# Kernel tuning notes

Hardware: AMD Instinct MI355X
Metric: run time of the kernel (lower is better)

The kernel has to match this reference:

```python
import jax, jax.numpy as jnp
import numpy as np

D = 1024
B = 16
T = 2048
LN_EPS = 1e-5


def setup_inputs() -> dict:
    key = jax.random.key(0)
    k_x, k_in, k_st = jax.random.split(key, 3)
    x = jax.random.normal(k_x, (B, T, D), dtype=jnp.float32)
    # nn.Linear(d, 2d, bias=False): weight [2D, D], y = x @ W.T
    s_in = 1.0 / np.sqrt(D)
    W_in = jax.random.uniform(k_in, (2 * D, D), dtype=jnp.float32, minval=-s_in, maxval=s_in)
    W_state = jax.random.uniform(k_st, (D, D), dtype=jnp.float32, minval=-s_in, maxval=s_in)
    gamma = jnp.ones((D,), dtype=jnp.float32)
    beta = jnp.zeros((D,), dtype=jnp.float32)
    return {"x": x, "W_in": W_in, "W_state": W_state, "gamma": gamma, "beta": beta}


def _glru(x, W_in, W_state, gamma, beta):
    # Batched projections over all timesteps (gates depend only on x).
    proj = jnp.einsum("btd,ed->bte", x, W_in)            # [B, T, 2D]
    gx, vx = jnp.split(proj, 2, axis=-1)                   # each [B, T, D]
    u = jax.nn.sigmoid(gx)                                  # [B, T, D]
    cand = jnp.einsum("btd,ed->bte", vx, W_state)        # [B, T, D]

    # Sequential diagonal linear recurrence: h_t = u_t * h_{t-1} + (1-u_t)*cand_t
    def step(h, uc):
        u_t, c_t = uc
        h = u_t * h + (1.0 - u_t) * c_t
        return h, h

    h0 = jnp.zeros((x.shape[0], x.shape[2]), dtype=x.dtype)
    us = jnp.swapaxes(u, 0, 1)       # [T, B, D]
    cs = jnp.swapaxes(cand, 0, 1)    # [T, B, D]
    _, ys = jax.lax.scan(step, h0, (us, cs))
    y = jnp.swapaxes(ys, 0, 1)       # [B, T, D]

    # LayerNorm over last dim
    mu = jnp.mean(y, axis=-1, keepdims=True)
    var = jnp.mean(jnp.square(y - mu), axis=-1, keepdims=True)
    return (y - mu) * jax.lax.rsqrt(var + LN_EPS) * gamma + beta


def reference(x, W_in, W_state, gamma, beta):
    return _glru(x, W_in, W_state, gamma, beta)
```

## Files before the change

### kernel.cpp

```cpp
#include <hip/hip_runtime.h>

#define D_DIM 1024
#define B_DIM 16
#define T_DIM 2048
#define M_TOT (B_DIM * T_DIM)
#define K_DIM 1024
#define LN_EPS 1e-5f
#define CHUNK 16
#define NCH (T_DIM / CHUNK)

typedef _Float16 half8 __attribute__((ext_vector_type(8)));
typedef _Float16 half4v __attribute__((ext_vector_type(4)));
typedef float f32x4 __attribute__((ext_vector_type(4)));

__global__ __launch_bounds__(256) void cvt_f32_f16(const float* __restrict__ in,
                                                   _Float16* __restrict__ out, int n8) {
    int i = blockIdx.x * blockDim.x + threadIdx.x;
    int stride = gridDim.x * blockDim.x;
    for (; i < n8; i += stride) {
        const float4* p = (const float4*)in + 2 * (size_t)i;
        float4 a = p[0], b = p[1];
        half8 h;
        h[0] = (_Float16)a.x; h[1] = (_Float16)a.y; h[2] = (_Float16)a.z; h[3] = (_Float16)a.w;
        h[4] = (_Float16)b.x; h[5] = (_Float16)b.y; h[6] = (_Float16)b.z; h[7] = (_Float16)b.w;
        ((half8*)out)[i] = h;
    }
}

__global__ __launch_bounds__(256) void transpose_cvt(const float* __restrict__ in,
                                                     _Float16* __restrict__ out) {
    __shared__ _Float16 t[32][33];
    int bx = blockIdx.x * 32, by = blockIdx.y * 32;
    int tx = threadIdx.x, ty = threadIdx.y;
#pragma unroll
    for (int j = 0; j < 4; ++j)
        t[ty + 8 * j][tx] = (_Float16)in[(size_t)(by + ty + 8 * j) * 1024 + bx + tx];
    __syncthreads();
#pragma unroll
    for (int j = 0; j < 4; ++j)
        out[(size_t)(bx + ty + 8 * j) * 1024 + by + tx] = t[tx][ty + 8 * j];
}

__device__ __forceinline__ void gl_lds16(const _Float16* g, _Float16* l) {
    __builtin_amdgcn_global_load_lds(
        (const __attribute__((address_space(1))) unsigned int*)g,
        (__attribute__((address_space(3))) unsigned int*)l,
        16, 0, 0);
}


__device__ __forceinline__ void stageA32(const _Float16* __restrict__ G,
                                         int row0, int kt,
                                         _Float16* lds0, int wid, int lane) {
#pragma unroll
    for (int call = 0; call < 2; ++call) {
        int c0 = call * 256 + wid * 64;
        int c  = c0 + lane;
        int rl = c >> 2;
        int cc = c & 3;
        int src = cc ^ ((rl >> 1) & 3);
        gl_lds16(G + (size_t)(row0 + rl) * 1024 + kt + src * 8,
                 lds0 + (size_t)c0 * 8);
    }
}

__device__ __forceinline__ void stageB32(const _Float16* __restrict__ G,
                                         int row0, int kt,
                                         _Float16* lds0, int wid, int lane) {
#pragma unroll
    for (int call = 0; call < 4; ++call) {
        int c0 = call * 256 + wid * 64;
        int c  = c0 + lane;
        int rl = c >> 2;
        int cc = c & 3;
        int src = cc ^ ((rl >> 1) & 3);
        gl_lds16(G + (size_t)(row0 + rl) * 1024 + kt + src * 8,
                 lds0 + (size_t)c0 * 8);
    }
}

__device__ __forceinline__ half8 frag32(const _Float16* base, int row, int kq) {
    int cc = kq ^ ((row >> 1) & 3);
    return *(const half8*)(base + (size_t)row * 32 + cc * 8);
}

template <int TB>
__device__ __forceinline__ void gstep(const _Float16* __restrict__ A,
                                      const _Float16* __restrict__ W,
                                      int m0, int nrow0, int t, int nkt,
                                      int wid, int lane, int wc, int r, int kq,
                                      _Float16 (&As)[3][128][32],
                                      _Float16 (&Bs)[3][256][32],
                                      f32x4 (&acc)[8][4]) {
    constexpr int NB = (TB + 2) % 3;
    half8 rb[4], ra0[4], ra1[4];

    if (t + 1 < nkt) asm volatile("s_waitcnt vmcnt(6)" ::: "memory");
    else             asm volatile("s_waitcnt vmcnt(0)" ::: "memory");
    __builtin_amdgcn_s_barrier();
    __builtin_amdgcn_sched_barrier(0);

#pragma unroll
    for (int ni = 0; ni < 4; ni++) rb[ni]  = frag32(&Bs[TB][0][0], wc * 64 + ni * 16 + r, kq);
#pragma unroll
    for (int mi = 0; mi < 4; mi++) ra0[mi] = frag32(&As[TB][0][0], mi * 16 + r, kq);
    if (t + 2 < nkt) {
        int kt2 = (t + 2) << 5;
        stageA32(A, m0,    kt2, &As[NB][0][0], wid, lane);
        stageB32(W, nrow0, kt2, &Bs[NB][0][0], wid, lane);
    }
    __builtin_amdgcn_s_setprio(1);
#pragma unroll
    for (int mi = 0; mi < 4; mi++)
#pragma unroll
        for (int ni = 0; ni < 4; ni++)
            acc[mi][ni] = __builtin_amdgcn_mfma_f32_16x16x32_f16(ra0[mi], rb[ni], acc[mi][ni], 0, 0, 0);
    __builtin_amdgcn_s_setprio(0);

#pragma unroll
    for (int mi = 0; mi < 4; mi++) ra1[mi] = frag32(&As[TB][0][0], 64 + mi * 16 + r, kq);
    __builtin_amdgcn_s_setprio(1);
#pragma unroll
    for (int mi = 0; mi < 4; mi++)
#pragma unroll
        for (int ni = 0; ni < 4; ni++)
            acc[4 + mi][ni] = __builtin_amdgcn_mfma_f32_16x16x32_f16(ra1[mi], rb[ni], acc[4 + mi][ni], 0, 0, 0);
    __builtin_amdgcn_s_setprio(0);
    __builtin_amdgcn_s_barrier();
}

__global__ __launch_bounds__(256, 2) void gemm256(const _Float16* __restrict__ A,
                                                  const _Float16* __restrict__ W,
                                                  _Float16* __restrict__ out0,
                                                  _Float16* __restrict__ out1) {
    __shared__ _Float16 As[3][128][32];
    __shared__ _Float16 Bs[3][256][32];

    int bid = blockIdx.x;
    int xcd = bid & 7, lin = bid >> 3;
    int mt = xcd * 32 + (lin >> 3);
    int nt = lin & 7;
    int m0 = mt * 128, nrow0 = nt * 256;

    int tid = threadIdx.x, wid = tid >> 6, lane = tid & 63;
    int wc = wid;
    int r = lane & 15, kq = lane >> 4;

    f32x4 acc[8][4];
#pragma unroll
    for (int i = 0; i < 8; i++)
#pragma unroll
        for (int j = 0; j < 4; j++) acc[i][j] = (f32x4)0.f;

    const int nkt = K_DIM >> 5;

    stageA32(A, m0,    0,  &As[0][0][0], wid, lane);
    stageB32(W, nrow0, 0,  &Bs[0][0][0], wid, lane);
    stageA32(A, m0,    32, &As[1][0][0], wid, lane);
    stageB32(W, nrow0, 32, &Bs[1][0][0], wid, lane);

    for (int t0 = 0; t0 < nkt; t0 += 3) {
        gstep<0>(A, W, m0, nrow0, t0, nkt, wid, lane, wc, r, kq, As, Bs, acc);
        if (t0 + 1 < nkt)
            gstep<1>(A, W, m0, nrow0, t0 + 1, nkt, wid, lane, wc, r, kq, As, Bs, acc);
        if (t0 + 2 < nkt)
            gstep<2>(A, W, m0, nrow0, t0 + 2, nkt, wid, lane, wc, r, kq, As, Bs, acc);
    }

    bool isGate = (nt < 4);
    _Float16* dst = isGate ? out0 : out1;
    int cb = (nt & 3) * 256 + wc * 64;
    int rr = kq * 4;
#pragma unroll
    for (int mi = 0; mi < 8; mi++) {
        int mbase = m0 + mi * 16 + rr;
#pragma unroll
        for (int ni = 0; ni < 4; ni++) {
            int n = cb + ni * 16 + r;
#pragma unroll
            for (int q = 0; q < 4; q++) {
                float v = acc[mi][ni][q];
                if (isGate) v = 1.f / (1.f + __expf(-v));
                dst[(size_t)(mbase + q) * D_DIM + n] = (_Float16)v;
            }
        }
    }
}

__global__ __launch_bounds__(256) void wcomb_splitk(const _Float16* __restrict__ A,
                                                    const _Float16* __restrict__ Bm,
                                                    float* __restrict__ part) {
    __shared__ _Float16 As[128 * 32];
    __shared__ _Float16 Bs[128 * 32];
    int bid = blockIdx.x;
    int mt = bid & 7, nt = (bid >> 3) & 7, sl = bid >> 6;
    int m0 = mt * 128, n0 = nt * 128, kbeg = sl * 256;
    int tid = threadIdx.x, wid = tid >> 6, lane = tid & 63;
    int wr = wid >> 1, wc = wid & 1;

    f32x4 acc[4][4];
#pragma unroll
    for (int i = 0; i < 4; i++)
#pragma unroll
        for (int j = 0; j < 4; j++) acc[i][j] = (f32x4)0.f;

    int r = lane & 15, kq = lane >> 4;

    for (int kt = kbeg; kt < kbeg + 256; kt += 32) {
        __syncthreads();
#pragma unroll
        for (int j = 0; j < 2; ++j) {
            int f = j * 256 + tid;
            int row = f >> 2, kc = f & 3;
            gl_lds16(A + (size_t)(m0 + row) * 1024 + kt + kc * 8, As + (size_t)(j * 256 + wid * 64) * 8);
            gl_lds16(Bm + (size_t)(n0 + row) * 1024 + kt + kc * 8, Bs + (size_t)(j * 256 + wid * 64) * 8);
        }
        __syncthreads();
        half8 af[4], bf[4];
#pragma unroll
        for (int mi = 0; mi < 4; mi++) af[mi] = *(const half8*)&As[(wr * 64 + mi * 16 + r) * 32 + kq * 8];
#pragma unroll
        for (int ni = 0; ni < 4; ni++) bf[ni] = *(const half8*)&Bs[(wc * 64 + ni * 16 + r) * 32 + kq * 8];
#pragma unroll
        for (int mi = 0; mi < 4; mi++)
#pragma unroll
            for (int ni = 0; ni < 4; ni++)
                acc[mi][ni] = __builtin_amdgcn_mfma_f32_16x16x32_f16(af[mi], bf[ni], acc[mi][ni], 0, 0, 0);
    }

    int rr = kq * 4;
    float* pbp = part + (size_t)sl * 1048576;
#pragma unroll
    for (int mi = 0; mi < 4; mi++) {
        int mbase = m0 + wr * 64 + mi * 16 + rr;
#pragma unroll
        for (int ni = 0; ni < 4; ni++) {
            int n = n0 + wc * 64 + ni * 16 + r;
#pragma unroll
            for (int q = 0; q < 4; q++)
                pbp[(size_t)(mbase + q) * 1024 + n] = acc[mi][ni][q];
        }
    }
}

__global__ __launch_bounds__(256) void wcomb_combine(const float* __restrict__ part,
                                                     _Float16* __restrict__ out) {
    int i = blockIdx.x * 256 + threadIdx.x;
    float4 s0 = ((const float4*)part)[i];
    float4 s1 = ((const float4*)(part + 1048576))[i];
    float4 s2 = ((const float4*)(part + 2097152))[i];
    float4 s3 = ((const float4*)(part + 3145728))[i];
    half4v o;
    o[0] = (_Float16)(s0.x + s1.x + s2.x + s3.x);
    o[1] = (_Float16)(s0.y + s1.y + s2.y + s3.y);
    o[2] = (_Float16)(s0.z + s1.z + s2.z + s3.z);
    o[3] = (_Float16)(s0.w + s1.w + s2.w + s3.w);
    ((half4v*)out)[i] = o;
}

__global__ __launch_bounds__(256) void scan_pass1(const _Float16* __restrict__ u,
                                                  const _Float16* __restrict__ cd,
                                                  float* __restrict__ Ac, float* __restrict__ Bc) {
    int idx = blockIdx.x * 256 + threadIdx.x;
    int dg = idx & 127, bc = idx >> 7;
    int b = bc >> 7, ch = bc & (NCH - 1);
    int d0 = dg * 8;
    size_t base = ((size_t)b * T_DIM + (size_t)ch * CHUNK) * D_DIM + d0;
    float Aa[8], Bb[8];
#pragma unroll
    for (int j = 0; j < 8; ++j) { Aa[j] = 1.f; Bb[j] = 0.f; }
#pragma unroll
    for (int t = 0; t < CHUNK; ++t) {
        half8 u8 = *(const half8*)&u[base + (size_t)t * D_DIM];
        half8 c8 = *(const half8*)&cd[base + (size_t)t * D_DIM];
#pragma unroll
        for (int j = 0; j < 8; ++j) {
            float ut = (float)u8[j], ct = (float)c8[j];
            Aa[j] *= ut;
            Bb[j] = fmaf(ut, Bb[j], (1.f - ut) * ct);
        }
    }
    size_t o = (size_t)bc * D_DIM + d0;
    *(float4*)&Ac[o]     = *(float4*)&Aa[0];
    *(float4*)&Ac[o + 4] = *(float4*)&Aa[4];
    *(float4*)&Bc[o]     = *(float4*)&Bb[0];
    *(float4*)&Bc[o + 4] = *(float4*)&Bb[4];
}

__global__ __launch_bounds__(256) void scan_pass2(float* __restrict__ AcH0,
                                                  const float* __restrict__ Bc) {
    int idx = blockIdx.x * 256 + threadIdx.x;
    int b = idx >> 10, d = idx & (D_DIM - 1);
    float h = 0.f;
#pragma unroll 8
    for (int ch = 0; ch < NCH; ++ch) {
        size_t k = ((size_t)(b * NCH + ch) << 10) + d;
        float a = AcH0[k];
        float bv = Bc[k];
        AcH0[k] = h;
        h = fmaf(a, h, bv);
    }
}

__global__ __launch_bounds__(64) void scan_ln(const _Float16* __restrict__ u,
                                              const _Float16* __restrict__ cd,
                                              const float* __restrict__ h0,
                                              const float* __restrict__ gamma,
                                              const float* __restrict__ beta,
                                              float* __restrict__ outp) {
    int bc = blockIdx.x;
    int b = bc >> 7, ch = bc & (NCH - 1);
    int lane = threadIdx.x;
    int d0 = lane * 16;
    size_t base = ((size_t)b * T_DIM + (size_t)ch * CHUNK) * D_DIM + d0;

    float g[16], be[16], h[16];
#pragma unroll
    for (int j = 0; j < 16; j += 4) {
        *(float4*)&g[j]  = *(const float4*)&gamma[d0 + j];
        *(float4*)&be[j] = *(const float4*)&beta[d0 + j];
    }
    size_t o = (size_t)bc * D_DIM + d0;
#pragma unroll
    for (int j = 0; j < 16; j += 4) *(float4*)&h[j] = *(const float4*)&h0[o + j];

    for (int t = 0; t < CHUNK; ++t) {
        size_t row = base + (size_t)t * D_DIM;
        half8 ua = *(const half8*)&u[row];
        half8 ub = *(const half8*)&u[row + 8];
        half8 ca = *(const half8*)&cd[row];
        half8 cb = *(const half8*)&cd[row + 8];
        float s = 0.f, q = 0.f;
#pragma unroll
        for (int j = 0; j < 8; ++j) {
            float ut = (float)ua[j], ct = (float)ca[j];
            h[j] = fmaf(ut, h[j] - ct, ct);
            s += h[j]; q += h[j] * h[j];
        }
#pragma unroll
        for (int j = 0; j < 8; ++j) {
            float ut = (float)ub[j], ct = (float)cb[j];
            h[8 + j] = fmaf(ut, h[8 + j] - ct, ct);
            s += h[8 + j]; q += h[8 + j] * h[8 + j];
        }
#pragma unroll
        for (int off = 32; off > 0; off >>= 1) {
            s += __shfl_xor(s, off);
            q += __shfl_xor(q, off);
        }
        float mu = s * (1.f / D_DIM);
        float var = q * (1.f / D_DIM) - mu * mu;
        float rs = rsqrtf(var + LN_EPS);
        float o16[16];
#pragma unroll
        for (int j = 0; j < 16; ++j) o16[j] = (h[j] - mu) * rs * g[j] + be[j];
#pragma unroll
        for (int j = 0; j < 16; j += 4) *(float4*)&outp[row + j] = *(float4*)&o16[j];
    }
}

extern "C" void kernel_launch(void* const* d_in, const int* in_sizes, int n_in,
                              void* d_out, int out_size, void* d_ws, size_t ws_size,
                              hipStream_t stream) {
    const float* x       = (const float*)d_in[0];
    const float* W_in    = (const float*)d_in[1];
    const float* W_state = (const float*)d_in[2];
    const float* gamma   = (const float*)d_in[3];
    const float* beta    = (const float*)d_in[4];
    float* out = (float*)d_out;

    char* w = (char*)d_ws;
    size_t off = 0;
    auto carve = [&](size_t bytes) {
        void* p = w + off;
        off += (bytes + 255) & ~(size_t)255;
        return p;
    };
    _Float16* xh   = (_Float16*)carve((size_t)M_TOT * K_DIM * 2);
    _Float16* Wall = (_Float16*)carve((size_t)2 * D_DIM * K_DIM * 2);
    _Float16* uarr = (_Float16*)carve((size_t)M_TOT * D_DIM * 2);
    _Float16* cand = (_Float16*)carve((size_t)M_TOT * D_DIM * 2);
    char* scratch  = (char*)carve((size_t)16 * 1024 * 1024);
    _Float16* wvxT = (_Float16*)scratch;
    _Float16* wst  = (_Float16*)(scratch + 2 * 1024 * 1024);
    float* Ac = (float*)scratch;
    float* Bc = (float*)(scratch + 8 * 1024 * 1024);
    float* wpart = (float*)cand;

    cvt_f32_f16<<<2048, 256, 0, stream>>>(x, xh, M_TOT * K_DIM / 8);
    cvt_f32_f16<<<512, 256, 0, stream>>>(W_in, Wall, D_DIM * K_DIM / 8);
    transpose_cvt<<<dim3(32, 32), dim3(32, 8), 0, stream>>>(W_in + (size_t)D_DIM * K_DIM, wvxT);
    cvt_f32_f16<<<512, 256, 0, stream>>>(W_state, wst, D_DIM * K_DIM / 8);

    wcomb_splitk<<<256, 256, 0, stream>>>(wst, wvxT, wpart);
    wcomb_combine<<<1024, 256, 0, stream>>>(wpart, Wall + (size_t)D_DIM * K_DIM);

    gemm256<<<2048, 256, 0, stream>>>(xh, Wall, uarr, cand);

    scan_pass1<<<(B_DIM * NCH * 128) / 256, 256, 0, stream>>>(uarr, cand, Ac, Bc);
    scan_pass2<<<(B_DIM * D_DIM) / 256, 256, 0, stream>>>(Ac, Bc);
    scan_ln<<<B_DIM * NCH, 64, 0, stream>>>(uarr, cand, Ac, gamma, beta, out);
}
```

Before: 308.2 us.

## Fuse x fp32-to-fp16 conversion into GEMM A-tile loading and merge weight prep kernels

Drops the separate pass that converts x to fp16. The GEMM now loads fp32 x tiles into registers, converts them, and writes them to a double-buffered LDS A tile, while B still streams through global_load_lds. The three weight-prep launches are also merged into one kernel. This removes a full read and write of the 64 MB-class x buffer and some launch overhead, but doubles the bytes the GEMM's A loads pull from global memory and adds register pressure and VALU conversion work to the inner loop.

```diff
diff --git a/kernel.cpp b/kernel.cpp
--- a/kernel.cpp
+++ b/kernel.cpp
@@ -13,32 +13,42 @@
 typedef _Float16 half4v __attribute__((ext_vector_type(4)));
 typedef float f32x4 __attribute__((ext_vector_type(4)));
 
-__global__ __launch_bounds__(256) void cvt_f32_f16(const float* __restrict__ in,
-                                                   _Float16* __restrict__ out, int n8) {
-    int i = blockIdx.x * blockDim.x + threadIdx.x;
-    int stride = gridDim.x * blockDim.x;
-    for (; i < n8; i += stride) {
-        const float4* p = (const float4*)in + 2 * (size_t)i;
-        float4 a = p[0], b = p[1];
+__global__ __launch_bounds__(256) void prep_w(const float* __restrict__ W_in,
+                                              const float* __restrict__ W_state,
+                                              _Float16* __restrict__ Wall,
+                                              _Float16* __restrict__ wvxT,
+                                              _Float16* __restrict__ wst) {
+    int b = blockIdx.x, tid = threadIdx.x;
+    if (b < 512) {
+        int i = b * 256 + tid;
+        const float4* p = (const float4*)W_in + 2 * (size_t)i;
+        float4 a = p[0], c = p[1];
         half8 h;
         h[0] = (_Float16)a.x; h[1] = (_Float16)a.y; h[2] = (_Float16)a.z; h[3] = (_Float16)a.w;
-        h[4] = (_Float16)b.x; h[5] = (_Float16)b.y; h[6] = (_Float16)b.z; h[7] = (_Float16)b.w;
-        ((half8*)out)[i] = h;
-    }
-}
-
-__global__ __launch_bounds__(256) void transpose_cvt(const float* __restrict__ in,
-                                                     _Float16* __restrict__ out) {
-    __shared__ _Float16 t[32][33];
-    int bx = blockIdx.x * 32, by = blockIdx.y * 32;
-    int tx = threadIdx.x, ty = threadIdx.y;
-#pragma unroll
-    for (int j = 0; j < 4; ++j)
-        t[ty + 8 * j][tx] = (_Float16)in[(size_t)(by + ty + 8 * j) * 1024 + bx + tx];
-    __syncthreads();
-#pragma unroll
-    for (int j = 0; j < 4; ++j)
-        out[(size_t)(bx + ty + 8 * j) * 1024 + by + tx] = t[tx][ty + 8 * j];
+        h[4] = (_Float16)c.x; h[5] = (_Float16)c.y; h[6] = (_Float16)c.z; h[7] = (_Float16)c.w;
+        ((half8*)Wall)[i] = h;
+    } else if (b < 1024) {
+        int i = (b - 512) * 256 + tid;
+        const float4* p = (const float4*)W_state + 2 * (size_t)i;
+        float4 a = p[0], c = p[1];
+        half8 h;
+        h[0] = (_Float16)a.x; h[1] = (_Float16)a.y; h[2] = (_Float16)a.z; h[3] = (_Float16)a.w;
+        h[4] = (_Float16)c.x; h[5] = (_Float16)c.y; h[6] = (_Float16)c.z; h[7] = (_Float16)c.w;
+        ((half8*)wst)[i] = h;
+    } else {
+        __shared__ _Float16 t[32][33];
+        int tile = b - 1024;
+        int bx = (tile & 31) * 32, by = (tile >> 5) * 32;
+        int tx = tid & 31, ty = tid >> 5;
+        const float* src = W_in + (size_t)D_DIM * K_DIM;
+#pragma unroll
+        for (int j = 0; j < 4; ++j)
+            t[ty + 8 * j][tx] = (_Float16)src[(size_t)(by + ty + 8 * j) * 1024 + bx + tx];
+        __syncthreads();
+#pragma unroll
+        for (int j = 0; j < 4; ++j)
+            wvxT[(size_t)(bx + ty + 8 * j) * 1024 + by + tx] = t[tx][ty + 8 * j];
+    }
 }
 
 __device__ __forceinline__ void gl_lds16(const _Float16* g, _Float16* l) {
@@ -48,21 +58,6 @@
         16, 0, 0);
 }
 
-
-__device__ __forceinline__ void stageA32(const _Float16* __restrict__ G,
-                                         int row0, int kt,
-                                         _Float16* lds0, int wid, int lane) {
-#pragma unroll
-    for (int call = 0; call < 2; ++call) {
-        int c0 = call * 256 + wid * 64;
-        int c  = c0 + lane;
-        int rl = c >> 2;
-        int cc = c & 3;
-        int src = cc ^ ((rl >> 1) & 3);
-        gl_lds16(G + (size_t)(row0 + rl) * 1024 + kt + src * 8,
-                 lds0 + (size_t)c0 * 8);
-    }
-}
 
 __device__ __forceinline__ void stageB32(const _Float16* __restrict__ G,
                                          int row0, int kt,
@@ -79,23 +74,53 @@
     }
 }
 
+__device__ __forceinline__ void ldA(const float* __restrict__ X, int m0, int kt,
+                                    int wid, int lane,
+                                    float4& p0, float4& p1, float4& p2, float4& p3) {
+    int c = wid * 64 + lane;
+    int rl = c >> 2, cc = c & 3;
+    int src = cc ^ ((rl >> 1) & 3);
+    const float* g = X + (size_t)(m0 + rl) * 1024 + kt + src * 8;
+    p0 = *(const float4*)g;
+    p1 = *(const float4*)(g + 4);
+    c = 256 + wid * 64 + lane;
+    rl = c >> 2; cc = c & 3; src = cc ^ ((rl >> 1) & 3);
+    g = X + (size_t)(m0 + rl) * 1024 + kt + src * 8;
+    p2 = *(const float4*)g;
+    p3 = *(const float4*)(g + 4);
+}
+
+__device__ __forceinline__ half8 cvt8(const float4& a, const float4& b) {
+    half8 h;
+    h[0] = (_Float16)a.x; h[1] = (_Float16)a.y; h[2] = (_Float16)a.z; h[3] = (_Float16)a.w;
+    h[4] = (_Float16)b.x; h[5] = (_Float16)b.y; h[6] = (_Float16)b.z; h[7] = (_Float16)b.w;
+    return h;
+}
+
+__device__ __forceinline__ void wrA(_Float16* lds0, int wid, int lane,
+                                    const float4& p0, const float4& p1,
+                                    const float4& p2, const float4& p3) {
+    *(half8*)(lds0 + (size_t)(wid * 64 + lane) * 8)       = cvt8(p0, p1);
+    *(half8*)(lds0 + (size_t)(256 + wid * 64 + lane) * 8) = cvt8(p2, p3);
+}
+
 __device__ __forceinline__ half8 frag32(const _Float16* base, int row, int kq) {
     int cc = kq ^ ((row >> 1) & 3);
     return *(const half8*)(base + (size_t)row * 32 + cc * 8);
 }
 
-template <int TB>
-__device__ __forceinline__ void gstep(const _Float16* __restrict__ A,
+template <int TA, int TB>
+__device__ __forceinline__ void gstep(const float* __restrict__ X,
                                       const _Float16* __restrict__ W,
                                       int m0, int nrow0, int t, int nkt,
                                       int wid, int lane, int wc, int r, int kq,
-                                      _Float16 (&As)[3][128][32],
+                                      _Float16 (&As)[2][128][32],
                                       _Float16 (&Bs)[3][256][32],
-                                      f32x4 (&acc)[8][4]) {
-    constexpr int NB = (TB + 2) % 3;
+                                      f32x4 (&acc)[8][4],
+                                      float4& l0, float4& l1, float4& l2, float4& l3) {
     half8 rb[4], ra0[4], ra1[4];
 
-    if (t + 1 < nkt) asm volatile("s_waitcnt vmcnt(6)" ::: "memory");
+    if (t + 1 < nkt) asm volatile("s_waitcnt vmcnt(4)" ::: "memory");
     else             asm volatile("s_waitcnt vmcnt(0)" ::: "memory");
     __builtin_amdgcn_s_barrier();
     __builtin_amdgcn_sched_barrier(0);
@@ -103,12 +128,12 @@
 #pragma unroll
     for (int ni = 0; ni < 4; ni++) rb[ni]  = frag32(&Bs[TB][0][0], wc * 64 + ni * 16 + r, kq);
 #pragma unroll
-    for (int mi = 0; mi < 4; mi++) ra0[mi] = frag32(&As[TB][0][0], mi * 16 + r, kq);
-    if (t + 2 < nkt) {
-        int kt2 = (t + 2) << 5;
-        stageA32(A, m0,    kt2, &As[NB][0][0], wid, lane);
-        stageB32(W, nrow0, kt2, &Bs[NB][0][0], wid, lane);
-    }
+    for (int mi = 0; mi < 4; mi++) ra0[mi] = frag32(&As[TA][0][0], mi * 16 + r, kq);
+
+    if (t + 1 < nkt) wrA(&As[TA ^ 1][0][0], wid, lane, l0, l1, l2, l3);
+    if (t + 2 < nkt) ldA(X, m0, (t + 2) << 5, wid, lane, l0, l1, l2, l3);
+    if (t + 2 < nkt) stageB32(W, nrow0, (t + 2) << 5, &Bs[(TB + 2) % 3][0][0], wid, lane);
+
     __builtin_amdgcn_s_setprio(1);
 #pragma unroll
     for (int mi = 0; mi < 4; mi++)
@@ -118,7 +143,7 @@
     __builtin_amdgcn_s_setprio(0);
 
 #pragma unroll
-    for (int mi = 0; mi < 4; mi++) ra1[mi] = frag32(&As[TB][0][0], 64 + mi * 16 + r, kq);
+    for (int mi = 0; mi < 4; mi++) ra1[mi] = frag32(&As[TA][0][0], 64 + mi * 16 + r, kq);
     __builtin_amdgcn_s_setprio(1);
 #pragma unroll
     for (int mi = 0; mi < 4; mi++)
@@ -126,14 +151,15 @@
         for (int ni = 0; ni < 4; ni++)
             acc[4 + mi][ni] = __builtin_amdgcn_mfma_f32_16x16x32_f16(ra1[mi], rb[ni], acc[4 + mi][ni], 0, 0, 0);
     __builtin_amdgcn_s_setprio(0);
+    asm volatile("s_waitcnt lgkmcnt(0)" ::: "memory");
     __builtin_amdgcn_s_barrier();
 }
 
-__global__ __launch_bounds__(256, 2) void gemm256(const _Float16* __restrict__ A,
+__global__ __launch_bounds__(256, 2) void gemm256(const float* __restrict__ X,
                                                   const _Float16* __restrict__ W,
                                                   _Float16* __restrict__ out0,
                                                   _Float16* __restrict__ out1) {
-    __shared__ _Float16 As[3][128][32];
+    __shared__ _Float16 As[2][128][32];
     __shared__ _Float16 Bs[3][256][32];
 
     int bid = blockIdx.x;
@@ -153,18 +179,23 @@
         for (int j = 0; j < 4; j++) acc[i][j] = (f32x4)0.f;
 
     const int nkt = K_DIM >> 5;
-
-    stageA32(A, m0,    0,  &As[0][0][0], wid, lane);
+    float4 l0, l1, l2, l3;
+
+    ldA(X, m0, 0, wid, lane, l0, l1, l2, l3);
+    asm volatile("s_waitcnt vmcnt(0)" ::: "memory");
+    wrA(&As[0][0][0], wid, lane, l0, l1, l2, l3);
     stageB32(W, nrow0, 0,  &Bs[0][0][0], wid, lane);
-    stageA32(A, m0,    32, &As[1][0][0], wid, lane);
+    ldA(X, m0, 32, wid, lane, l0, l1, l2, l3);
     stageB32(W, nrow0, 32, &Bs[1][0][0], wid, lane);
-
-    for (int t0 = 0; t0 < nkt; t0 += 3) {
-        gstep<0>(A, W, m0, nrow0, t0, nkt, wid, lane, wc, r, kq, As, Bs, acc);
-        if (t0 + 1 < nkt)
-            gstep<1>(A, W, m0, nrow0, t0 + 1, nkt, wid, lane, wc, r, kq, As, Bs, acc);
-        if (t0 + 2 < nkt)
-            gstep<2>(A, W, m0, nrow0, t0 + 2, nkt, wid, lane, wc, r, kq, As, Bs, acc);
+    asm volatile("s_waitcnt lgkmcnt(0)" ::: "memory");
+
+    for (int t0 = 0; t0 < nkt; t0 += 6) {
+        gstep<0, 0>(X, W, m0, nrow0, t0,     nkt, wid, lane, wc, r, kq, As, Bs, acc, l0, l1, l2, l3);
+        if (t0 + 1 < nkt) gstep<1, 1>(X, W, m0, nrow0, t0 + 1, nkt, wid, lane, wc, r, kq, As, Bs, acc, l0, l1, l2, l3);
+        if (t0 + 2 < nkt) gstep<0, 2>(X, W, m0, nrow0, t0 + 2, nkt, wid, lane, wc, r, kq, As, Bs, acc, l0, l1, l2, l3);
+        if (t0 + 3 < nkt) gstep<1, 0>(X, W, m0, nrow0, t0 + 3, nkt, wid, lane, wc, r, kq, As, Bs, acc, l0, l1, l2, l3);
+        if (t0 + 4 < nkt) gstep<0, 1>(X, W, m0, nrow0, t0 + 4, nkt, wid, lane, wc, r, kq, As, Bs, acc, l0, l1, l2, l3);
+        if (t0 + 5 < nkt) gstep<1, 2>(X, W, m0, nrow0, t0 + 5, nkt, wid, lane, wc, r, kq, As, Bs, acc, l0, l1, l2, l3);
     }
 
     bool isGate = (nt < 4);
@@ -376,7 +407,6 @@
         off += (bytes + 255) & ~(size_t)255;
         return p;
     };
-    _Float16* xh   = (_Float16*)carve((size_t)M_TOT * K_DIM * 2);
     _Float16* Wall = (_Float16*)carve((size_t)2 * D_DIM * K_DIM * 2);
     _Float16* uarr = (_Float16*)carve((size_t)M_TOT * D_DIM * 2);
     _Float16* cand = (_Float16*)carve((size_t)M_TOT * D_DIM * 2);
@@ -387,15 +417,12 @@
     float* Bc = (float*)(scratch + 8 * 1024 * 1024);
     float* wpart = (float*)cand;
 
-    cvt_f32_f16<<<2048, 256, 0, stream>>>(x, xh, M_TOT * K_DIM / 8);
-    cvt_f32_f16<<<512, 256, 0, stream>>>(W_in, Wall, D_DIM * K_DIM / 8);
-    transpose_cvt<<<dim3(32, 32), dim3(32, 8), 0, stream>>>(W_in + (size_t)D_DIM * K_DIM, wvxT);
-    cvt_f32_f16<<<512, 256, 0, stream>>>(W_state, wst, D_DIM * K_DIM / 8);
+    prep_w<<<2048, 256, 0, stream>>>(W_in, W_state, Wall, wvxT, wst);
 
     wcomb_splitk<<<256, 256, 0, stream>>>(wst, wvxT, wpart);
     wcomb_combine<<<1024, 256, 0, stream>>>(wpart, Wall + (size_t)D_DIM * K_DIM);
 
-    gemm256<<<2048, 256, 0, stream>>>(xh, Wall, uarr, cand);
+    gemm256<<<2048, 256, 0, stream>>>(x, Wall, uarr, cand);
 
     scan_pass1<<<(B_DIM * NCH * 128) / 256, 256, 0, stream>>>(uarr, cand, Ac, Bc);
     scan_pass2<<<(B_DIM * D_DIM) / 256, 256, 0, stream>>>(Ac, Bc);
```

Result: faster. 296.1 us (-3.9%).

## Fuse chunk scan pass1 into GEMM epilogue and merge prep kernels

Applied to the files above, without the earlier changes.

The GEMM B tile now interleaves gate and candidate rows for the same 128 channels, so each block holds matching u and cand values. The epilogue computes each 16-step chunk's scan coefficients (A, B) in registers using cross-lane shuffles, which removes the separate scan_pass1 kernel and its re-read of u and cand. The four input conversion and transpose kernels are also merged into one launch. The costs are a heavier epilogue with extra shuffles and some branch divergence in the combined prep kernel.

```diff
diff --git a/kernel.cpp b/kernel.cpp
--- a/kernel.cpp
+++ b/kernel.cpp
@@ -13,32 +13,54 @@
 typedef _Float16 half4v __attribute__((ext_vector_type(4)));
 typedef float f32x4 __attribute__((ext_vector_type(4)));
 
-__global__ __launch_bounds__(256) void cvt_f32_f16(const float* __restrict__ in,
-                                                   _Float16* __restrict__ out, int n8) {
-    int i = blockIdx.x * blockDim.x + threadIdx.x;
-    int stride = gridDim.x * blockDim.x;
-    for (; i < n8; i += stride) {
-        const float4* p = (const float4*)in + 2 * (size_t)i;
-        float4 a = p[0], b = p[1];
+__global__ __launch_bounds__(256) void prep_all(const float* __restrict__ x,
+                                                const float* __restrict__ W_in,
+                                                const float* __restrict__ W_state,
+                                                _Float16* __restrict__ xh,
+                                                _Float16* __restrict__ Wall,
+                                                _Float16* __restrict__ wvxT,
+                                                _Float16* __restrict__ wst) {
+    __shared__ _Float16 t[32][33];
+    int b = blockIdx.x, tid = threadIdx.x;
+    if (b < 2048) {
+        int i = b * 256 + tid;
+        for (; i < M_TOT * K_DIM / 8; i += 2048 * 256) {
+            const float4* p = (const float4*)x + 2 * (size_t)i;
+            float4 a = p[0], c = p[1];
+            half8 h;
+            h[0] = (_Float16)a.x; h[1] = (_Float16)a.y; h[2] = (_Float16)a.z; h[3] = (_Float16)a.w;
+            h[4] = (_Float16)c.x; h[5] = (_Float16)c.y; h[6] = (_Float16)c.z; h[7] = (_Float16)c.w;
+            ((half8*)xh)[i] = h;
+        }
+    } else if (b < 2560) {
+        int i = (b - 2048) * 256 + tid;
+        const float4* p = (const float4*)W_in + 2 * (size_t)i;
+        float4 a = p[0], c = p[1];
         half8 h;
         h[0] = (_Float16)a.x; h[1] = (_Float16)a.y; h[2] = (_Float16)a.z; h[3] = (_Float16)a.w;
-        h[4] = (_Float16)b.x; h[5] = (_Float16)b.y; h[6] = (_Float16)b.z; h[7] = (_Float16)b.w;
-        ((half8*)out)[i] = h;
-    }
-}
-
-__global__ __launch_bounds__(256) void transpose_cvt(const float* __restrict__ in,
-                                                     _Float16* __restrict__ out) {
-    __shared__ _Float16 t[32][33];
-    int bx = blockIdx.x * 32, by = blockIdx.y * 32;
-    int tx = threadIdx.x, ty = threadIdx.y;
-#pragma unroll
-    for (int j = 0; j < 4; ++j)
-        t[ty + 8 * j][tx] = (_Float16)in[(size_t)(by + ty + 8 * j) * 1024 + bx + tx];
-    __syncthreads();
-#pragma unroll
-    for (int j = 0; j < 4; ++j)
-        out[(size_t)(bx + ty + 8 * j) * 1024 + by + tx] = t[tx][ty + 8 * j];
+        h[4] = (_Float16)c.x; h[5] = (_Float16)c.y; h[6] = (_Float16)c.z; h[7] = (_Float16)c.w;
+        ((half8*)Wall)[i] = h;
+    } else if (b < 3072) {
+        int i = (b - 2560) * 256 + tid;
+        const float4* p = (const float4*)W_state + 2 * (size_t)i;
+        float4 a = p[0], c = p[1];
+        half8 h;
+        h[0] = (_Float16)a.x; h[1] = (_Float16)a.y; h[2] = (_Float16)a.z; h[3] = (_Float16)a.w;
+        h[4] = (_Float16)c.x; h[5] = (_Float16)c.y; h[6] = (_Float16)c.z; h[7] = (_Float16)c.w;
+        ((half8*)wst)[i] = h;
+    } else {
+        int tile = b - 3072;
+        int bx = (tile & 31) * 32, by = (tile >> 5) * 32;
+        int tx = tid & 31, ty = tid >> 5;
+        const float* src = W_in + (size_t)D_DIM * K_DIM;
+#pragma unroll
+        for (int j = 0; j < 4; ++j)
+            t[ty + 8 * j][tx] = (_Float16)src[(size_t)(by + ty + 8 * j) * 1024 + bx + tx];
+        __syncthreads();
+#pragma unroll
+        for (int j = 0; j < 4; ++j)
+            wvxT[(size_t)(bx + ty + 8 * j) * 1024 + by + tx] = t[tx][ty + 8 * j];
+    }
 }
 
 __device__ __forceinline__ void gl_lds16(const _Float16* g, _Float16* l) {
@@ -65,7 +87,7 @@
 }
 
 __device__ __forceinline__ void stageB32(const _Float16* __restrict__ G,
-                                         int row0, int kt,
+                                         int nt, int kt,
                                          _Float16* lds0, int wid, int lane) {
 #pragma unroll
     for (int call = 0; call < 4; ++call) {
@@ -74,7 +96,8 @@
         int rl = c >> 2;
         int cc = c & 3;
         int src = cc ^ ((rl >> 1) & 3);
-        gl_lds16(G + (size_t)(row0 + rl) * 1024 + kt + src * 8,
+        int row = nt * 128 + (rl & 127) + ((rl >> 7) << 10);
+        gl_lds16(G + (size_t)row * 1024 + kt + src * 8,
                  lds0 + (size_t)c0 * 8);
     }
 }
@@ -87,7 +110,7 @@
 template <int TB>
 __device__ __forceinline__ void gstep(const _Float16* __restrict__ A,
                                       const _Float16* __restrict__ W,
-                                      int m0, int nrow0, int t, int nkt,
+                                      int m0, int nt, int t, int nkt,
                                       int wid, int lane, int wc, int r, int kq,
                                       _Float16 (&As)[3][128][32],
                                       _Float16 (&Bs)[3][256][32],
@@ -101,13 +124,14 @@
     __builtin_amdgcn_sched_barrier(0);
 
 #pragma unroll
-    for (int ni = 0; ni < 4; ni++) rb[ni]  = frag32(&Bs[TB][0][0], wc * 64 + ni * 16 + r, kq);
+    for (int ni = 0; ni < 4; ni++)
+        rb[ni] = frag32(&Bs[TB][0][0], (ni >> 1) * 128 + wc * 32 + (ni & 1) * 16 + r, kq);
 #pragma unroll
     for (int mi = 0; mi < 4; mi++) ra0[mi] = frag32(&As[TB][0][0], mi * 16 + r, kq);
     if (t + 2 < nkt) {
         int kt2 = (t + 2) << 5;
-        stageA32(A, m0,    kt2, &As[NB][0][0], wid, lane);
-        stageB32(W, nrow0, kt2, &Bs[NB][0][0], wid, lane);
+        stageA32(A, m0, kt2, &As[NB][0][0], wid, lane);
+        stageB32(W, nt, kt2, &Bs[NB][0][0], wid, lane);
     }
     __builtin_amdgcn_s_setprio(1);
 #pragma unroll
@@ -131,8 +155,10 @@
 
 __global__ __launch_bounds__(256, 2) void gemm256(const _Float16* __restrict__ A,
                                                   const _Float16* __restrict__ W,
-                                                  _Float16* __restrict__ out0,
-                                                  _Float16* __restrict__ out1) {
+                                                  _Float16* __restrict__ out_u,
+                                                  _Float16* __restrict__ out_c,
+                                                  float* __restrict__ Ac,
+                                                  float* __restrict__ Bc) {
     __shared__ _Float16 As[3][128][32];
     __shared__ _Float16 Bs[3][256][32];
 
@@ -140,7 +166,7 @@
     int xcd = bid & 7, lin = bid >> 3;
     int mt = xcd * 32 + (lin >> 3);
     int nt = lin & 7;
-    int m0 = mt * 128, nrow0 = nt * 256;
+    int m0 = mt * 128;
 
     int tid = threadIdx.x, wid = tid >> 6, lane = tid & 63;
     int wc = wid;
@@ -154,34 +180,52 @@
 
     const int nkt = K_DIM >> 5;
 
-    stageA32(A, m0,    0,  &As[0][0][0], wid, lane);
-    stageB32(W, nrow0, 0,  &Bs[0][0][0], wid, lane);
-    stageA32(A, m0,    32, &As[1][0][0], wid, lane);
-    stageB32(W, nrow0, 32, &Bs[1][0][0], wid, lane);
+    stageA32(A, m0, 0,  &As[0][0][0], wid, lane);
+    stageB32(W, nt, 0,  &Bs[0][0][0], wid, lane);
+    stageA32(A, m0, 32, &As[1][0][0], wid, lane);
+    stageB32(W, nt, 32, &Bs[1][0][0], wid, lane);
 
     for (int t0 = 0; t0 < nkt; t0 += 3) {
-        gstep<0>(A, W, m0, nrow0, t0, nkt, wid, lane, wc, r, kq, As, Bs, acc);
+        gstep<0>(A, W, m0, nt, t0, nkt, wid, lane, wc, r, kq, As, Bs, acc);
         if (t0 + 1 < nkt)
-            gstep<1>(A, W, m0, nrow0, t0 + 1, nkt, wid, lane, wc, r, kq, As, Bs, acc);
+            gstep<1>(A, W, m0, nt, t0 + 1, nkt, wid, lane, wc, r, kq, As, Bs, acc);
         if (t0 + 2 < nkt)
-            gstep<2>(A, W, m0, nrow0, t0 + 2, nkt, wid, lane, wc, r, kq, As, Bs, acc);
-    }
-
-    bool isGate = (nt < 4);
-    _Float16* dst = isGate ? out0 : out1;
-    int cb = (nt & 3) * 256 + wc * 64;
+            gstep<2>(A, W, m0, nt, t0 + 2, nkt, wid, lane, wc, r, kq, As, Bs, acc);
+    }
+
     int rr = kq * 4;
 #pragma unroll
     for (int mi = 0; mi < 8; mi++) {
         int mbase = m0 + mi * 16 + rr;
-#pragma unroll
-        for (int ni = 0; ni < 4; ni++) {
-            int n = cb + ni * 16 + r;
+        float Aab[2] = {1.f, 1.f}, Bab[2] = {0.f, 0.f};
+#pragma unroll
+        for (int ni = 0; ni < 2; ni++) {
+            int d = nt * 128 + wc * 32 + ni * 16 + r;
 #pragma unroll
             for (int q = 0; q < 4; q++) {
-                float v = acc[mi][ni][q];
-                if (isGate) v = 1.f / (1.f + __expf(-v));
-                dst[(size_t)(mbase + q) * D_DIM + n] = (_Float16)v;
+                float u = 1.f / (1.f + __expf(-acc[mi][ni][q]));
+                float c = acc[mi][ni + 2][q];
+                size_t m = (size_t)(mbase + q);
+                out_u[m * D_DIM + d] = (_Float16)u;
+                out_c[m * D_DIM + d] = (_Float16)c;
+                Bab[ni] = fmaf(u, Bab[ni], (1.f - u) * c);
+                Aab[ni] *= u;
+            }
+        }
+#pragma unroll
+        for (int ni = 0; ni < 2; ni++) {
+            float Aa = Aab[ni], Bb = Bab[ni];
+            float oA = __shfl_xor(Aa, 16), oB = __shfl_xor(Bb, 16);
+            if (kq & 1) { Bb = fmaf(Aa, oB, Bb); Aa *= oA; }
+            else        { Bb = fmaf(oA, Bb, oB); Aa *= oA; }
+            oA = __shfl_xor(Aa, 32); oB = __shfl_xor(Bb, 32);
+            if (kq & 2) { Bb = fmaf(Aa, oB, Bb); Aa *= oA; }
+            else        { Bb = fmaf(oA, Bb, oB); Aa *= oA; }
+            if (kq == 0) {
+                int d = nt * 128 + wc * 32 + ni * 16 + r;
+                int bc = mt * 8 + mi;
+                Ac[(size_t)bc * 1024 + d] = Aa;
+                Bc[(size_t)bc * 1024 + d] = Bb;
             }
         }
     }
@@ -256,35 +300,6 @@
     o[2] = (_Float16)(s0.z + s1.z + s2.z + s3.z);
     o[3] = (_Float16)(s0.w + s1.w + s2.w + s3.w);
     ((half4v*)out)[i] = o;
-}
-
-__global__ __launch_bounds__(256) void scan_pass1(const _Float16* __restrict__ u,
-                                                  const _Float16* __restrict__ cd,
-                                                  float* __restrict__ Ac, float* __restrict__ Bc) {
-    int idx = blockIdx.x * 256 + threadIdx.x;
-    int dg = idx & 127, bc = idx >> 7;
-    int b = bc >> 7, ch = bc & (NCH - 1);
-    int d0 = dg * 8;
-    size_t base = ((size_t)b * T_DIM + (size_t)ch * CHUNK) * D_DIM + d0;
-    float Aa[8], Bb[8];
-#pragma unroll
-    for (int j = 0; j < 8; ++j) { Aa[j] = 1.f; Bb[j] = 0.f; }
-#pragma unroll
-    for (int t = 0; t < CHUNK; ++t) {
-        half8 u8 = *(const half8*)&u[base + (size_t)t * D_DIM];
-        half8 c8 = *(const half8*)&cd[base + (size_t)t * D_DIM];
-#pragma unroll
-        for (int j = 0; j < 8; ++j) {
-            float ut = (float)u8[j], ct = (float)c8[j];
-            Aa[j] *= ut;
-            Bb[j] = fmaf(ut, Bb[j], (1.f - ut) * ct);
-        }
-    }
-    size_t o = (size_t)bc * D_DIM + d0;
-    *(float4*)&Ac[o]     = *(float4*)&Aa[0];
-    *(float4*)&Ac[o + 4] = *(float4*)&Aa[4];
-    *(float4*)&Bc[o]     = *(float4*)&Bb[0];
-    *(float4*)&Bc[o + 4] = *(float4*)&Bb[4];
 }
 
 __global__ __launch_bounds__(256) void scan_pass2(float* __restrict__ AcH0,
@@ -387,17 +402,13 @@
     float* Bc = (float*)(scratch + 8 * 1024 * 1024);
     float* wpart = (float*)cand;
 
-    cvt_f32_f16<<<2048, 256, 0, stream>>>(x, xh, M_TOT * K_DIM / 8);
-    cvt_f32_f16<<<512, 256, 0, stream>>>(W_in, Wall, D_DIM * K_DIM / 8);
-    transpose_cvt<<<dim3(32, 32), dim3(32, 8), 0, stream>>>(W_in + (size_t)D_DIM * K_DIM, wvxT);
-    cvt_f32_f16<<<512, 256, 0, stream>>>(W_state, wst, D_DIM * K_DIM / 8);
+    prep_all<<<4096, 256, 0, stream>>>(x, W_in, W_state, xh, Wall, wvxT, wst);
 
     wcomb_splitk<<<256, 256, 0, stream>>>(wst, wvxT, wpart);
     wcomb_combine<<<1024, 256, 0, stream>>>(wpart, Wall + (size_t)D_DIM * K_DIM);
 
-    gemm256<<<2048, 256, 0, stream>>>(xh, Wall, uarr, cand);
-
-    scan_pass1<<<(B_DIM * NCH * 128) / 256, 256, 0, stream>>>(uarr, cand, Ac, Bc);
+    gemm256<<<2048, 256, 0, stream>>>(xh, Wall, uarr, cand, Ac, Bc);
+
     scan_pass2<<<(B_DIM * D_DIM) / 256, 256, 0, stream>>>(Ac, Bc);
     scan_ln<<<B_DIM * NCH, 64, 0, stream>>>(uarr, cand, Ac, gamma, beta, out);
 }
```

New measurement: 300.9 us. -2.4%, faster.
